# Kernel tuning notes

Hardware: AMD Instinct MI355X
Metric: run time of the kernel (lower is better)

The kernel has to match this reference:

```python
import jax, jax.numpy as jnp
import numpy as np

N = 100_000   # nodes
D = 128       # emb_size
E = 1_600_000 # edges (avg degree 16)
K = 64        # K1 (channel 0 pooling clusters)
LAYERS = 2


def _l2norm(x):
    # F.normalize(x, dim=-1, p=2) with eps=1e-12
    return x / jnp.maximum(jnp.linalg.norm(x, axis=-1, keepdims=True), 1e-12)


def setup_inputs() -> dict:
    key = jax.random.key(0)
    ks = jax.random.split(key, 9)
    return {
        "adj": jax.random.uniform(ks[0], (N,), dtype=jnp.float32),
        "edge_row": jax.random.randint(ks[1], (E,), 0, N),
        "edge_col": jax.random.randint(ks[2], (E,), 0, N),
        "edge_val": jax.random.uniform(ks[3], (E,), dtype=jnp.float32),
        "embedding": jax.random.normal(ks[4], (N, D), dtype=jnp.float32) * 0.02,
        "W_item0": jax.random.normal(ks[5], (D, D), dtype=jnp.float32) * 0.05,
        "W_item1": jax.random.normal(ks[6], (D, D), dtype=jnp.float32) * 0.05,
        "W_i1": jax.random.normal(ks[7], (D, D), dtype=jnp.float32) * 0.05,
        "W_i2": jax.random.normal(ks[8], (D, K), dtype=jnp.float32) * 0.05,
        "channel": 0,
    }


def reference(adj, edge_row, edge_col, edge_val, embedding,
              W_item0, W_item1, W_i1, W_i2, channel):
    n = adj.shape[0]

    def spmm(x):  # sparse [N,N] @ dense [N,D] via COO gather + segment_sum
        return jax.ops.segment_sum(edge_val[:, None] * x[edge_col], edge_row,
                                   num_segments=n)

    x = embedding
    final = [x]
    finalh = []
    for W in (W_item0, W_item1):  # structurally distinct per-layer weights
        x = spmm(x @ W)                                   # [N,D]
        H1 = jax.nn.relu(x @ W_i1 + x)                    # [N,D]
        H1 = jax.nn.softmax(H1 @ W_i2, axis=1)            # [N,K]
        h = H1.T * adj                                    # [K,N]
        h = h * (1.0 / (jnp.sum(h, axis=0) + 1e-8))       # column-normalize
        h = H1 @ (h @ x)                                  # [N,K]@[K,D] -> [N,D]
        x = h + x
        final.append(_l2norm(x))
        finalh.append(_l2norm(h))
    item_embeddings = sum(final) / (LAYERS + 1)
    hs = sum(finalh) / LAYERS
    return item_embeddings, hs
```

## Files before the change

kernel.cpp:

```cpp
#include <hip/hip_runtime.h>

constexpr int DD = 128;
constexpr int KK = 64;
constexpr int NBLK_C2 = 512;
constexpr int CH = 512;

typedef __attribute__((ext_vector_type(8))) short bf16x8;
typedef __attribute__((ext_vector_type(4))) float f32x4;

union U4 { unsigned u[4]; int4 i4; bf16x8 v; };

__device__ inline unsigned bf16_rne(float x) {
  unsigned u = __float_as_uint(x);
  u += 0x7fff + ((u >> 16) & 1);
  return u >> 16;
}
__device__ inline float bf16f(unsigned h) { return __uint_as_float(h << 16); }
__device__ inline void split2(float a, float b, unsigned& hi, unsigned& lo) {
  const unsigned h0 = bf16_rne(a), h1 = bf16_rne(b);
  const unsigned l0 = bf16_rne(a - bf16f(h0)), l1 = bf16_rne(b - bf16f(h1));
  hi = h0 | (h1 << 16);
  lo = l0 | (l1 << 16);
}

__global__ void k_prepW(const float* __restrict__ W, unsigned* __restrict__ Whi,
                        unsigned* __restrict__ Wlo) {
  const int id = blockIdx.x * 256 + threadIdx.x;
  const int j = id & 3, l = (id >> 2) & 63, t = (id >> 8) & 7, ks = id >> 11;
  const int k0 = 32 * ks + 8 * (l >> 4) + 2 * j;
  const int col = 16 * t + (l & 15);
  const float e0 = W[k0 * 128 + col], e1 = W[(k0 + 1) * 128 + col];
  unsigned hi, lo;
  split2(e0, e1, hi, lo);
  Whi[id] = hi;
  Wlo[id] = lo;
}

__global__ void k_prepWs(const float* __restrict__ W, unsigned* __restrict__ Wf) {
  const int id = blockIdx.x * 256 + threadIdx.x;
  const int j = id & 3, l = (id >> 2) & 63, t = (id >> 8) & 3, ks = id >> 10;
  const int k0 = 32 * ks + 8 * (l >> 4) + 2 * j;
  const int col = 16 * t + (l & 15);
  const unsigned h0 = bf16_rne(W[k0 * 64 + col]);
  const unsigned h1 = bf16_rne(W[(k0 + 1) * 64 + col]);
  Wf[id] = h0 | (h1 << 16);
}

__global__ void k_prepM(const float* __restrict__ M, unsigned* __restrict__ Mhi,
                        unsigned* __restrict__ Mlo) {
  const int id = blockIdx.x * 256 + threadIdx.x;
  const int j = id & 3, l = (id >> 2) & 63, t = (id >> 8) & 7, ks = id >> 11;
  const int k0 = 32 * ks + 8 * (l >> 4) + 2 * j;
  const int col = 16 * t + (l & 15);
  unsigned hi, lo;
  split2(M[k0 * 128 + col], M[(k0 + 1) * 128 + col], hi, lo);
  Mhi[id] = hi;
  Mlo[id] = lo;
}

__global__ __launch_bounds__(512) void k_gemm_mfma(const float* __restrict__ X,
                                                   const unsigned* __restrict__ Whi,
                                                   const unsigned* __restrict__ Wlo,
                                                   unsigned short* __restrict__ Yb,
                                                   int n) {
  __shared__ unsigned sb[2 * 8192];
  {
    const int t = threadIdx.x;
    uint4* d0 = (uint4*)sb;
    const uint4* s0 = (const uint4*)Whi;
#pragma unroll
    for (int i = 0; i < 4; ++i) d0[t + 512 * i] = s0[t + 512 * i];
    uint4* d1 = (uint4*)(sb + 8192);
    const uint4* s1 = (const uint4*)Wlo;
#pragma unroll
    for (int i = 0; i < 4; ++i) d1[t + 512 * i] = s1[t + 512 * i];
  }
  __syncthreads();
  const int wave = threadIdx.x >> 6, lane = threadIdx.x & 63;
  const int l15 = lane & 15, lhi = lane >> 4;
  const int row0 = blockIdx.x * 256 + wave * 32;
  if (row0 >= n) return;
  f32x4 acc[2][8];
#pragma unroll
  for (int rt = 0; rt < 2; ++rt)
#pragma unroll
    for (int t = 0; t < 8; ++t) acc[rt][t] = (f32x4){0.f, 0.f, 0.f, 0.f};
#pragma unroll
  for (int ks = 0; ks < 4; ++ks) {
    U4 ah[2], al[2];
#pragma unroll
    for (int rt = 0; rt < 2; ++rt) {
      int r = row0 + rt * 16 + l15;
      if (r >= n) r = n - 1;
      const float4 x0 = *(const float4*)&X[(size_t)r * DD + ks * 32 + lhi * 8];
      const float4 x1 = *(const float4*)&X[(size_t)r * DD + ks * 32 + lhi * 8 + 4];
      split2(x0.x, x0.y, ah[rt].u[0], al[rt].u[0]);
      split2(x0.z, x0.w, ah[rt].u[1], al[rt].u[1]);
      split2(x1.x, x1.y, ah[rt].u[2], al[rt].u[2]);
      split2(x1.z, x1.w, ah[rt].u[3], al[rt].u[3]);
    }
#pragma unroll
    for (int t = 0; t < 8; ++t) {
      U4 bh, bl;
      const int off = ((ks * 8 + t) * 64 + lane) * 4;
      bh.i4 = *(const int4*)&sb[off];
      bl.i4 = *(const int4*)&sb[8192 + off];
#pragma unroll
      for (int rt = 0; rt < 2; ++rt) {
        acc[rt][t] = __builtin_amdgcn_mfma_f32_16x16x32_bf16(ah[rt].v, bh.v, acc[rt][t], 0, 0, 0);
        acc[rt][t] = __builtin_amdgcn_mfma_f32_16x16x32_bf16(al[rt].v, bh.v, acc[rt][t], 0, 0, 0);
        acc[rt][t] = __builtin_amdgcn_mfma_f32_16x16x32_bf16(ah[rt].v, bl.v, acc[rt][t], 0, 0, 0);
      }
    }
  }
#pragma unroll
  for (int rt = 0; rt < 2; ++rt)
#pragma unroll
    for (int rr = 0; rr < 4; ++rr) {
      const int row = row0 + rt * 16 + lhi * 4 + rr;
      if (row < n) {
#pragma unroll
        for (int t = 0; t < 8; ++t)
          Yb[(size_t)row * DD + t * 16 + l15] =
              (unsigned short)bf16_rne(acc[rt][t][rr]);
      }
    }
}

__global__ void k_hist(const int* __restrict__ er, int* __restrict__ cnt, int E) {
  for (long e = (long)blockIdx.x * blockDim.x + threadIdx.x; e < E;
       e += (long)gridDim.x * blockDim.x)
    atomicAdd(&cnt[er[e]], 1);
}

__global__ __launch_bounds__(256) void k_chunksum(const int* __restrict__ cnt,
                                                  int* __restrict__ csum, int n) {
  const int c = blockIdx.x, t = threadIdx.x;
  const int i0 = c * CH + 2 * t;
  int s2 = 0;
  if (i0 < n) s2 += cnt[i0];
  if (i0 + 1 < n) s2 += cnt[i0 + 1];
#pragma unroll
  for (int off = 32; off >= 1; off >>= 1) s2 += __shfl_xor(s2, off);
  __shared__ int ws_[4];
  if ((t & 63) == 0) ws_[t >> 6] = s2;
  __syncthreads();
  if (t == 0) csum[c] = ws_[0] + ws_[1] + ws_[2] + ws_[3];
}

__global__ __launch_bounds__(256) void k_chunkscan(const int* __restrict__ csum,
                                                   int* __restrict__ coff, int nch) {
  __shared__ int s[256];
  const int t = threadIdx.x;
  const int v = (t < nch) ? csum[t] : 0;
  s[t] = v;
  __syncthreads();
  for (int off = 1; off < 256; off <<= 1) {
    const int u = (t >= off) ? s[t - off] : 0;
    __syncthreads();
    s[t] += u;
    __syncthreads();
  }
  coff[t] = s[t] - v;
}

__global__ __launch_bounds__(256) void k_rowptr(const int* __restrict__ cnt,
                                                const int* __restrict__ coff,
                                                int* __restrict__ rowptr,
                                                int n, int E) {
  const int c = blockIdx.x, t = threadIdx.x;
  const int i0 = c * CH + 2 * t, i1 = i0 + 1;
  const int v0 = (i0 < n) ? cnt[i0] : 0;
  const int v1 = (i1 < n) ? cnt[i1] : 0;
  __shared__ int s[256];
  const int s2 = v0 + v1;
  s[t] = s2;
  __syncthreads();
  for (int off = 1; off < 256; off <<= 1) {
    const int u = (t >= off) ? s[t - off] : 0;
    __syncthreads();
    s[t] += u;
    __syncthreads();
  }
  const int excl = s[t] - s2 + coff[c];
  if (i0 < n) rowptr[i0] = excl;
  if (i1 < n) rowptr[i1] = excl + v0;
  if (c == 0 && t == 0) rowptr[n] = E;
}

__global__ void k_scatter(const int* __restrict__ er, const int* __restrict__ ec,
                          const float* __restrict__ ev,
                          const int* __restrict__ rowptr, int* __restrict__ cur,
                          int2* __restrict__ erec, int E, int n) {
  const int rng = blockIdx.x & 7;
  const int g = blockIdx.x >> 3;
  const long e_lo = (long)g * E / 256;
  const long e_hi = (long)(g + 1) * E / 256;
  const int r_lo = (int)((long)rng * n / 8);
  const int r_hi = (int)((long)(rng + 1) * n / 8);
  for (long e = e_lo + threadIdx.x; e < e_hi; e += 256) {
    const int r = er[e];
    if (r >= r_lo && r < r_hi) {
      const int pos = rowptr[r] + atomicAdd(&cur[r], 1);
      erec[pos] = make_int2(ec[e], __float_as_int(ev[e]));
    }
  }
}

__global__ __launch_bounds__(256) void k_spmm_csr(const int* __restrict__ rowptr,
                                                  const int2* __restrict__ erec,
                                                  const unsigned* __restrict__ Yb,
                                                  float* __restrict__ Xo, int n) {
  const int lane = threadIdx.x & 63;
  const int c0 = 2 * lane;
  const long gw = (long)blockIdx.x * 4 + (threadIdx.x >> 6);
  const long nw = (long)gridDim.x * 4;
  for (long row = gw; row < n; row += nw) {
    const int b = rowptr[row], e2 = rowptr[row + 1];
    float a0 = 0.f, a1 = 0.f, b0 = 0.f, b1 = 0.f;
    float c00 = 0.f, c1 = 0.f, d0 = 0.f, d1 = 0.f;
    int e = b;
    for (; e + 4 <= e2; e += 4) {
      const int2 r0 = erec[e], r1 = erec[e + 1];
      const int2 r2 = erec[e + 2], r3 = erec[e + 3];
      const unsigned q0 = Yb[(size_t)r0.x * (DD / 2) + lane];
      const unsigned q1 = Yb[(size_t)r1.x * (DD / 2) + lane];
      const unsigned q2 = Yb[(size_t)r2.x * (DD / 2) + lane];
      const unsigned q3 = Yb[(size_t)r3.x * (DD / 2) + lane];
      const float v0 = __int_as_float(r0.y), v1 = __int_as_float(r1.y);
      const float v2 = __int_as_float(r2.y), v3 = __int_as_float(r3.y);
      a0 = fmaf(v0, __uint_as_float(q0 << 16), a0);
      a1 = fmaf(v0, __uint_as_float(q0 & 0xffff0000u), a1);
      b0 = fmaf(v1, __uint_as_float(q1 << 16), b0);
      b1 = fmaf(v1, __uint_as_float(q1 & 0xffff0000u), b1);
      c00 = fmaf(v2, __uint_as_float(q2 << 16), c00);
      c1 = fmaf(v2, __uint_as_float(q2 & 0xffff0000u), c1);
      d0 = fmaf(v3, __uint_as_float(q3 << 16), d0);
      d1 = fmaf(v3, __uint_as_float(q3 & 0xffff0000u), d1);
    }
    for (; e + 2 <= e2; e += 2) {
      const int2 r0 = erec[e], r1 = erec[e + 1];
      const float v0 = __int_as_float(r0.y), v1 = __int_as_float(r1.y);
      const unsigned q0 = Yb[(size_t)r0.x * (DD / 2) + lane];
      const unsigned q1 = Yb[(size_t)r1.x * (DD / 2) + lane];
      a0 = fmaf(v0, __uint_as_float(q0 << 16), a0);
      a1 = fmaf(v0, __uint_as_float(q0 & 0xffff0000u), a1);
      b0 = fmaf(v1, __uint_as_float(q1 << 16), b0);
      b1 = fmaf(v1, __uint_as_float(q1 & 0xffff0000u), b1);
    }
    if (e < e2) {
      const int2 r0 = erec[e];
      const float v = __int_as_float(r0.y);
      const unsigned q = Yb[(size_t)r0.x * (DD / 2) + lane];
      a0 = fmaf(v, __uint_as_float(q << 16), a0);
      a1 = fmaf(v, __uint_as_float(q & 0xffff0000u), a1);
    }
    *(float2*)&Xo[(size_t)row * DD + c0] =
        make_float2((a0 + b0) + (c00 + d0), (a1 + b1) + (c1 + d1));
  }
}

__global__ __launch_bounds__(512) void k_c1_mfma(const float* __restrict__ X,
                                                 const unsigned* __restrict__ W1hi,
                                                 const unsigned* __restrict__ W1lo,
                                                 const unsigned* __restrict__ W2f,
                                                 const float* __restrict__ adj,
                                                 float* __restrict__ H1g,
                                                 float* __restrict__ trow, int n) {
  __shared__ unsigned s1[2 * 8192];
  __shared__ unsigned s2[4096];
  __shared__ unsigned h1s[8 * 16 * 68];
  {
    const int t = threadIdx.x;
    uint4* d0 = (uint4*)s1;
    const uint4* sA = (const uint4*)W1hi;
    const uint4* sB = (const uint4*)W1lo;
#pragma unroll
    for (int i = 0; i < 4; ++i) d0[t + 512 * i] = sA[t + 512 * i];
    uint4* d1 = (uint4*)(s1 + 8192);
#pragma unroll
    for (int i = 0; i < 4; ++i) d1[t + 512 * i] = sB[t + 512 * i];
    uint4* d2 = (uint4*)s2;
    const uint4* sC = (const uint4*)W2f;
#pragma unroll
    for (int i = 0; i < 2; ++i) d2[t + 512 * i] = sC[t + 512 * i];
  }
  __syncthreads();
  const int wave = threadIdx.x >> 6, lane = threadIdx.x & 63;
  const int l15 = lane & 15, lhi = lane >> 4;
  unsigned* __restrict__ h1w = h1s + wave * (16 * 68);
  const int row0 = blockIdx.x * 128 + wave * 16;
  if (row0 >= n) return;

  U4 ah[4], al[4];
#pragma unroll
  for (int ks = 0; ks < 4; ++ks) {
    int r = row0 + l15;
    if (r >= n) r = n - 1;
    const float4 x0 = *(const float4*)&X[(size_t)r * DD + ks * 32 + lhi * 8];
    const float4 x1 = *(const float4*)&X[(size_t)r * DD + ks * 32 + lhi * 8 + 4];
    split2(x0.x, x0.y, ah[ks].u[0], al[ks].u[0]);
    split2(x0.z, x0.w, ah[ks].u[1], al[ks].u[1]);
    split2(x1.x, x1.y, ah[ks].u[2], al[ks].u[2]);
    split2(x1.z, x1.w, ah[ks].u[3], al[ks].u[3]);
  }
  f32x4 acc1[8];
#pragma unroll
  for (int t = 0; t < 8; ++t) acc1[t] = (f32x4){0.f, 0.f, 0.f, 0.f};
#pragma unroll
  for (int ks = 0; ks < 4; ++ks) {
#pragma unroll
    for (int t = 0; t < 8; ++t) {
      U4 bh, bl;
      const int off = ((ks * 8 + t) * 64 + lane) * 4;
      bh.i4 = *(const int4*)&s1[off];
      bl.i4 = *(const int4*)&s1[8192 + off];
      acc1[t] = __builtin_amdgcn_mfma_f32_16x16x32_bf16(ah[ks].v, bh.v, acc1[t], 0, 0, 0);
      acc1[t] = __builtin_amdgcn_mfma_f32_16x16x32_bf16(al[ks].v, bh.v, acc1[t], 0, 0, 0);
      acc1[t] = __builtin_amdgcn_mfma_f32_16x16x32_bf16(ah[ks].v, bl.v, acc1[t], 0, 0, 0);
    }
  }

  unsigned short* __restrict__ h16 = (unsigned short*)h1w;
#pragma unroll
  for (int rr = 0; rr < 4; ++rr) {
    int row = row0 + 4 * lhi + rr;
    if (row >= n) row = n - 1;
    const float* __restrict__ xr = X + (size_t)row * DD;
#pragma unroll
    for (int t = 0; t < 8; ++t) {
      float v = acc1[t][rr] + xr[16 * t + l15];
      v = fmaxf(v, 0.f);
      h16[(4 * lhi + rr) * 136 + 16 * t + l15] = (unsigned short)bf16_rne(v);
    }
  }

  f32x4 acc3[4];
#pragma unroll
  for (int t = 0; t < 4; ++t) acc3[t] = (f32x4){0.f, 0.f, 0.f, 0.f};
#pragma unroll
  for (int ks = 0; ks < 4; ++ks) {
    U4 a3;
    a3.i4 = *(const int4*)&h1w[l15 * 68 + ks * 16 + lhi * 4];
#pragma unroll
    for (int t = 0; t < 4; ++t) {
      U4 b3;
      b3.i4 = *(const int4*)&s2[((ks * 4 + t) * 64 + lane) * 4];
      acc3[t] = __builtin_amdgcn_mfma_f32_16x16x32_bf16(a3.v, b3.v, acc3[t], 0, 0, 0);
    }
  }

#pragma unroll
  for (int rr = 0; rr < 4; ++rr) {
    const int row = row0 + 4 * lhi + rr;
    float z0 = acc3[0][rr], z1 = acc3[1][rr], z2 = acc3[2][rr], z3 = acc3[3][rr];
    float m = fmaxf(fmaxf(z0, z1), fmaxf(z2, z3));
#pragma unroll
    for (int off = 8; off >= 1; off >>= 1) m = fmaxf(m, __shfl_xor(m, off));
    const float p0 = expf(z0 - m), p1 = expf(z1 - m);
    const float p2 = expf(z2 - m), p3 = expf(z3 - m);
    float s = p0 + p1 + p2 + p3;
#pragma unroll
    for (int off = 8; off >= 1; off >>= 1) s += __shfl_xor(s, off);
    const float inv = 1.0f / s;
    if (row < n) {
      float* __restrict__ hr = H1g + (size_t)row * KK;
      hr[l15] = p0 * inv;
      hr[16 + l15] = p1 * inv;
      hr[32 + l15] = p2 * inv;
      hr[48 + l15] = p3 * inv;
      if (l15 == 0) {
        const float a = adj[row];
        trow[row] = a / (a + 1e-8f);
      }
    }
  }
}

__global__ __launch_bounds__(1024, 4) void k_c2(const float* __restrict__ X,
                                                const float* __restrict__ trow,
                                                const float* __restrict__ H1g,
                                                float* __restrict__ Mpart, int n) {
  __shared__ float cmb[3 * 4 * 16 * 2 * 64];
  const int t = threadIdx.x;
  const int wave = t >> 6, lane = t & 63;
  const int rg = wave >> 2, kg = wave & 3;
  const int kb = kg * 16;
  const int d0 = 2 * lane;
  float macc[16][2];
#pragma unroll
  for (int j = 0; j < 16; ++j) { macc[j][0] = 0.f; macc[j][1] = 0.f; }
  const int bx = blockIdx.x;
  for (long row = (long)bx + 512L * rg; row < n; row += 2048L) {
    const int r = __builtin_amdgcn_readfirstlane((int)row);
    const float tr = trow[r];
    const float2 xv = *(const float2*)&X[(size_t)r * DD + d0];
    const float px0 = tr * xv.x, px1 = tr * xv.y;
    const float* __restrict__ hrow = H1g + (size_t)r * KK + kb;
#pragma unroll
    for (int j = 0; j < 16; ++j) {
      const float hj = hrow[j];
      macc[j][0] = fmaf(hj, px0, macc[j][0]);
      macc[j][1] = fmaf(hj, px1, macc[j][1]);
    }
  }
  if (rg > 0) {
    float* __restrict__ dst = cmb + ((rg - 1) * 4 + kg) * (16 * 2 * 64);
#pragma unroll
    for (int j = 0; j < 16; ++j) {
      dst[(2 * j + 0) * 64 + lane] = macc[j][0];
      dst[(2 * j + 1) * 64 + lane] = macc[j][1];
    }
  }
  __syncthreads();
  if (rg == 0) {
#pragma unroll
    for (int g = 0; g < 3; ++g) {
      const float* __restrict__ src = cmb + (g * 4 + kg) * (16 * 2 * 64);
#pragma unroll
      for (int j = 0; j < 16; ++j) {
        macc[j][0] += src[(2 * j + 0) * 64 + lane];
        macc[j][1] += src[(2 * j + 1) * 64 + lane];
      }
    }
    float* __restrict__ mp = Mpart + (size_t)bx * (KK * DD);
#pragma unroll
    for (int j = 0; j < 16; ++j)
      *(float2*)&mp[(kb + j) * DD + d0] = make_float2(macc[j][0], macc[j][1]);
  }
}

__global__ void k_dred1(const float* __restrict__ Mpart, float* __restrict__ Mp2) {
  const int j = blockIdx.x * blockDim.x + threadIdx.x;
  const int i = j & (KK * DD - 1);
  const int c = j >> 13;
  float s = 0.f;
#pragma unroll
  for (int q = 0; q < 16; ++q)
    s += Mpart[(size_t)(c * 16 + q) * (KK * DD) + i];
  Mp2[(size_t)c * (KK * DD) + i] = s;
}

__global__ void k_dred2(const float* __restrict__ Mp2, float* __restrict__ Mg) {
  const int i = blockIdx.x * blockDim.x + threadIdx.x;
  float s = 0.f;
#pragma unroll
  for (int c = 0; c < 32; ++c) s += Mp2[(size_t)c * (KK * DD) + i];
  Mg[i] = s;
}

__global__ __launch_bounds__(512) void k_fin_mfma(const float* __restrict__ H1g,
                                                  const unsigned* __restrict__ Mhi,
                                                  const unsigned* __restrict__ Mlo,
                                                  const float* __restrict__ emb,
                                                  float* __restrict__ Xb,
                                                  float* __restrict__ out,
                                                  int n, int first) {
  __shared__ unsigned sm[2 * 4096];
  {
    const int t = threadIdx.x;
    uint4* d0 = (uint4*)sm;
    const uint4* s0 = (const uint4*)Mhi;
#pragma unroll
    for (int i = 0; i < 2; ++i) d0[t + 512 * i] = s0[t + 512 * i];
    uint4* d1 = (uint4*)(sm + 4096);
    const uint4* s1 = (const uint4*)Mlo;
#pragma unroll
    for (int i = 0; i < 2; ++i) d1[t + 512 * i] = s1[t + 512 * i];
  }
  __syncthreads();
  const int wave = threadIdx.x >> 6, lane = threadIdx.x & 63;
  const int l15 = lane & 15, lhi = lane >> 4;
  const size_t hoff = (size_t)n * DD;
  const int row0 = blockIdx.x * 128 + wave * 16;
  if (row0 >= n) return;

  U4 ah[2], al[2];
  {
    int ra = row0 + l15;
    if (ra >= n) ra = n - 1;
    const float* __restrict__ hp = H1g + (size_t)ra * KK;
#pragma unroll
    for (int ks = 0; ks < 2; ++ks) {
      const float4 x0 = *(const float4*)&hp[ks * 32 + lhi * 8];
      const float4 x1 = *(const float4*)&hp[ks * 32 + lhi * 8 + 4];
      split2(x0.x, x0.y, ah[ks].u[0], al[ks].u[0]);
      split2(x0.z, x0.w, ah[ks].u[1], al[ks].u[1]);
      split2(x1.x, x1.y, ah[ks].u[2], al[ks].u[2]);
      split2(x1.z, x1.w, ah[ks].u[3], al[ks].u[3]);
    }
  }
  f32x4 acc[8];
#pragma unroll
  for (int t = 0; t < 8; ++t) acc[t] = (f32x4){0.f, 0.f, 0.f, 0.f};
#pragma unroll
  for (int ks = 0; ks < 2; ++ks) {
#pragma unroll
    for (int t = 0; t < 8; ++t) {
      U4 bh, bl;
      const int off = ((ks * 8 + t) * 64 + lane) * 4;
      bh.i4 = *(const int4*)&sm[off];
      bl.i4 = *(const int4*)&sm[4096 + off];
      acc[t] = __builtin_amdgcn_mfma_f32_16x16x32_bf16(ah[ks].v, bh.v, acc[t], 0, 0, 0);
      acc[t] = __builtin_amdgcn_mfma_f32_16x16x32_bf16(al[ks].v, bh.v, acc[t], 0, 0, 0);
      acc[t] = __builtin_amdgcn_mfma_f32_16x16x32_bf16(ah[ks].v, bl.v, acc[t], 0, 0, 0);
    }
  }
#pragma unroll
  for (int rr = 0; rr < 4; ++rr) {
    const int row = row0 + 4 * lhi + rr;
    const int rc = (row < n) ? row : (n - 1);
    float hh[8], xx[8];
    float sh = 0.f, sx = 0.f;
#pragma unroll
    for (int t = 0; t < 8; ++t) {
      const float xv = Xb[(size_t)rc * DD + 16 * t + l15];
      hh[t] = acc[t][rr];
      xx[t] = hh[t] + xv;
      sh = fmaf(hh[t], hh[t], sh);
      sx = fmaf(xx[t], xx[t], sx);
    }
#pragma unroll
    for (int off = 8; off >= 1; off >>= 1) {
      sh += __shfl_xor(sh, off);
      sx += __shfl_xor(sx, off);
    }
    const float ih = 0.5f / fmaxf(sqrtf(sh), 1e-12f);
    const float ix = (1.0f / 3.0f) / fmaxf(sqrtf(sx), 1e-12f);
    if (row < n) {
#pragma unroll
      for (int t = 0; t < 8; ++t) {
        const size_t oi = (size_t)row * DD + 16 * t + l15;
        Xb[oi] = xx[t];
        float ci, ch;
        if (first) {
          ci = emb[oi] * (1.0f / 3.0f);
          ch = 0.f;
        } else {
          ci = out[oi];
          ch = out[hoff + oi];
        }
        out[oi] = ci + xx[t] * ix;
        out[hoff + oi] = ch + hh[t] * ih;
      }
    }
  }
}

extern "C" void kernel_launch(void* const* d_in, const int* in_sizes, int n_in,
                              void* d_out, int out_size, void* d_ws, size_t ws_size,
                              hipStream_t stream) {
  const float* adj  = (const float*)d_in[0];
  const int*   erow = (const int*)d_in[1];
  const int*   ecol = (const int*)d_in[2];
  const float* eval = (const float*)d_in[3];
  const float* emb  = (const float*)d_in[4];
  const float* W0   = (const float*)d_in[5];
  const float* W1   = (const float*)d_in[6];
  const float* Wi1  = (const float*)d_in[7];
  const float* Wi2  = (const float*)d_in[8];
  const int n = in_sizes[0];
  const int E = in_sizes[1];
  float* out = (float*)d_out;

  float* xb    = (float*)d_ws;
  float* yb    = xb + (size_t)n * DD;
  unsigned short* Ybf = (unsigned short*)yb;
  float* H1g   = yb + (size_t)n * (DD / 2);
  float* Mpart = H1g + (size_t)n * KK;
  float* Mp2   = Mpart + (size_t)NBLK_C2 * KK * DD;
  float* Mg    = Mp2 + (size_t)32 * KK * DD;
  int*   cnt    = (int*)(Mg + KK * DD);
  int*   rowptr = cnt + n;
  int*   csum   = rowptr + n + 4;
  int*   coff   = csum + 256;
  int2*  erec   = (int2*)(coff + 256);
  float* trow   = (float*)(erec + E);
  unsigned* w0hi  = (unsigned*)(trow + n);
  unsigned* w0lo  = w0hi + 8192;
  unsigned* w1hi_ = w0lo + 8192;
  unsigned* w1lo_ = w1hi_ + 8192;
  unsigned* wi1hi = w1lo_ + 8192;
  unsigned* wi1lo = wi1hi + 8192;
  unsigned* wi2f  = wi1lo + 8192;
  unsigned* mhi   = wi2f + 4096;
  unsigned* mlo   = mhi + 4096;

  const int NCH = (n + CH - 1) / CH;

  k_prepW<<<32, 256, 0, stream>>>(W0, w0hi, w0lo);
  k_prepW<<<32, 256, 0, stream>>>(W1, w1hi_, w1lo_);
  k_prepW<<<32, 256, 0, stream>>>(Wi1, wi1hi, wi1lo);
  k_prepWs<<<16, 256, 0, stream>>>(Wi2, wi2f);

  hipMemsetAsync(cnt, 0, (size_t)n * sizeof(int), stream);
  k_hist<<<2048, 256, 0, stream>>>(erow, cnt, E);
  k_chunksum<<<NCH, 256, 0, stream>>>(cnt, csum, n);
  k_chunkscan<<<1, 256, 0, stream>>>(csum, coff, NCH);
  k_rowptr<<<NCH, 256, 0, stream>>>(cnt, coff, rowptr, n, E);
  hipMemsetAsync(cnt, 0, (size_t)n * sizeof(int), stream);
  k_scatter<<<2048, 256, 0, stream>>>(erow, ecol, eval, rowptr, cnt, erec, E, n);

  const int g_gm  = (n + 255) / 256;
  const int g_c1m = (n + 127) / 128;
  const int g_fin = (n + 127) / 128;

  for (int L = 0; L < 2; ++L) {
    const unsigned* Whi = (L == 0) ? w0hi : w1hi_;
    const unsigned* Wlo = (L == 0) ? w0lo : w1lo_;
    const float* Xin = (L == 0) ? emb : xb;
    k_gemm_mfma<<<g_gm, 512, 0, stream>>>(Xin, Whi, Wlo, Ybf, n);
    k_spmm_csr<<<2048, 256, 0, stream>>>(rowptr, erec, (const unsigned*)Ybf, xb, n);
    k_c1_mfma<<<g_c1m, 512, 0, stream>>>(xb, wi1hi, wi1lo, wi2f, adj, H1g, trow, n);
    k_c2<<<NBLK_C2, 1024, 0, stream>>>(xb, trow, H1g, Mpart, n);
    k_dred1<<<1024, 256, 0, stream>>>(Mpart, Mp2);
    k_dred2<<<32, 256, 0, stream>>>(Mp2, Mg);
    k_prepM<<<16, 256, 0, stream>>>(Mg, mhi, mlo);
    k_fin_mfma<<<g_fin, 512, 0, stream>>>(H1g, mhi, mlo, emb, xb, out, n, (L == 0) ? 1 : 0);
  }
}
```

Baseline: 711.0 us.

## Build CSR via two-pass shared-memory bucketing and deepen SpMM unroll to 8

Replaces the 8-way row-range-filtered atomic scatter with a two-pass bucket sort. The first pass bins edges into 512-row buckets in shared memory and flushes them in chunks to a scratch buffer aliased onto xb. The second pass places each bucket's edges into their final CSR slots using shared-memory atomics. This cuts the repeated reads of the edge arrays and the scattered global atomics, at the cost of an extra pass and a bit-packed column/local-row encoding that assumes columns fit in 20 bits. The SpMM inner loop is also unrolled to 8 independent gathers to raise memory-level parallelism, which uses more registers.

Measured after the change: 720.5 us. No clear change (+1.3%).

```diff
diff --git a/kernel.cpp b/kernel.cpp
--- a/kernel.cpp
+++ b/kernel.cpp
@@ -4,6 +4,8 @@
 constexpr int KK = 64;
 constexpr int NBLK_C2 = 512;
 constexpr int CH = 512;
+constexpr int NBK = 256;
+constexpr int BCAP = 32;
 
 typedef __attribute__((ext_vector_type(8))) short bf16x8;
 typedef __attribute__((ext_vector_type(4))) float f32x4;
@@ -188,22 +190,88 @@
   if (c == 0 && t == 0) rowptr[n] = E;
 }
 
-__global__ void k_scatter(const int* __restrict__ er, const int* __restrict__ ec,
-                          const float* __restrict__ ev,
-                          const int* __restrict__ rowptr, int* __restrict__ cur,
-                          int2* __restrict__ erec, int E, int n) {
-  const int rng = blockIdx.x & 7;
-  const int g = blockIdx.x >> 3;
-  const long e_lo = (long)g * E / 256;
-  const long e_hi = (long)(g + 1) * E / 256;
-  const int r_lo = (int)((long)rng * n / 8);
-  const int r_hi = (int)((long)(rng + 1) * n / 8);
-  for (long e = e_lo + threadIdx.x; e < e_hi; e += 256) {
-    const int r = er[e];
-    if (r >= r_lo && r < r_hi) {
-      const int pos = rowptr[r] + atomicAdd(&cur[r], 1);
-      erec[pos] = make_int2(ec[e], __float_as_int(ev[e]));
-    }
+__global__ __launch_bounds__(256) void k_bucketA(const int* __restrict__ er,
+                                                 const int* __restrict__ ec,
+                                                 const float* __restrict__ ev,
+                                                 const int* __restrict__ rowptr,
+                                                 int* __restrict__ gcur,
+                                                 int2* __restrict__ gbuf,
+                                                 int E, int nbk) {
+  __shared__ int2 buf[NBK * BCAP];
+  __shared__ int cnt[NBK];
+  const int t = threadIdx.x;
+  for (int i = t; i < NBK; i += 256) cnt[i] = 0;
+  __syncthreads();
+  const long e_lo = (long)blockIdx.x * E / 512;
+  const long e_hi = (long)(blockIdx.x + 1) * E / 512;
+  for (long s = e_lo; s < e_hi; s += 2048) {
+    const long s_end = (s + 2048 < e_hi) ? (s + 2048) : e_hi;
+    unsigned pend = 0;
+#pragma unroll
+    for (int k = 0; k < 8; ++k) {
+      const long e = s + t + 256 * k;
+      if (e < s_end) {
+        const int r = er[e];
+        const int b = r >> 9;
+        const int p = atomicAdd(&cnt[b], 1);
+        if (p < BCAP)
+          buf[b * BCAP + p] = make_int2(ec[e] | ((r & 511) << 20), __float_as_int(ev[e]));
+        else
+          pend |= 1u << k;
+      }
+    }
+    __syncthreads();
+    if (t < nbk) {
+      const int m = min(cnt[t], BCAP);
+      if (m > 0) {
+        const int base = rowptr[t << 9] + atomicAdd(&gcur[t], m);
+        for (int i = 0; i < m; ++i) gbuf[base + i] = buf[t * BCAP + i];
+      }
+      cnt[t] = 0;
+    }
+    __syncthreads();
+    while (pend) {
+      const int k = __ffs(pend) - 1;
+      pend &= pend - 1;
+      const long e = s + t + 256 * k;
+      const int r = er[e];
+      const int b = r >> 9;
+      const int2 rec = make_int2(ec[e] | ((r & 511) << 20), __float_as_int(ev[e]));
+      const int p = atomicAdd(&cnt[b], 1);
+      if (p < BCAP) {
+        buf[b * BCAP + p] = rec;
+      } else {
+        const int base = rowptr[b << 9] + atomicAdd(&gcur[b], 1);
+        gbuf[base] = rec;
+      }
+    }
+  }
+  __syncthreads();
+  if (t < nbk) {
+    const int m = min(cnt[t], BCAP);
+    if (m > 0) {
+      const int base = rowptr[t << 9] + atomicAdd(&gcur[t], m);
+      for (int i = 0; i < m; ++i) gbuf[base + i] = buf[t * BCAP + i];
+    }
+  }
+}
+
+__global__ __launch_bounds__(512) void k_bucketB(const int2* __restrict__ gbuf,
+                                                 const int* __restrict__ rowptr,
+                                                 int2* __restrict__ erec, int n) {
+  __shared__ int cur[512];
+  const int b = blockIdx.x, t = threadIdx.x;
+  cur[t] = 0;
+  __syncthreads();
+  const int r_lo = b << 9;
+  const int r_hi = (r_lo + 512 < n) ? (r_lo + 512) : n;
+  const int g_lo = rowptr[r_lo], g_hi = rowptr[r_hi];
+  for (int i = g_lo + t; i < g_hi; i += 512) {
+    const int2 rec = gbuf[i];
+    const int rl = ((unsigned)rec.x) >> 20;
+    const int col = rec.x & 0xFFFFF;
+    const int pos = rowptr[r_lo + rl] + atomicAdd(&cur[rl], 1);
+    erec[pos] = make_int2(col, rec.y);
   }
 }
 
@@ -217,46 +285,44 @@
   const long nw = (long)gridDim.x * 4;
   for (long row = gw; row < n; row += nw) {
     const int b = rowptr[row], e2 = rowptr[row + 1];
-    float a0 = 0.f, a1 = 0.f, b0 = 0.f, b1 = 0.f;
-    float c00 = 0.f, c1 = 0.f, d0 = 0.f, d1 = 0.f;
+    float a0[8], a1[8];
+#pragma unroll
+    for (int i = 0; i < 8; ++i) { a0[i] = 0.f; a1[i] = 0.f; }
     int e = b;
-    for (; e + 4 <= e2; e += 4) {
+    for (; e + 8 <= e2; e += 8) {
+      int2 rr[8];
+      unsigned qq[8];
+#pragma unroll
+      for (int i = 0; i < 8; ++i) rr[i] = erec[e + i];
+#pragma unroll
+      for (int i = 0; i < 8; ++i) qq[i] = Yb[(size_t)rr[i].x * (DD / 2) + lane];
+#pragma unroll
+      for (int i = 0; i < 8; ++i) {
+        const float v = __int_as_float(rr[i].y);
+        a0[i] = fmaf(v, __uint_as_float(qq[i] << 16), a0[i]);
+        a1[i] = fmaf(v, __uint_as_float(qq[i] & 0xffff0000u), a1[i]);
+      }
+    }
+    for (; e + 2 <= e2; e += 2) {
       const int2 r0 = erec[e], r1 = erec[e + 1];
-      const int2 r2 = erec[e + 2], r3 = erec[e + 3];
       const unsigned q0 = Yb[(size_t)r0.x * (DD / 2) + lane];
       const unsigned q1 = Yb[(size_t)r1.x * (DD / 2) + lane];
-      const unsigned q2 = Yb[(size_t)r2.x * (DD / 2) + lane];
-      const unsigned q3 = Yb[(size_t)r3.x * (DD / 2) + lane];
       const float v0 = __int_as_float(r0.y), v1 = __int_as_float(r1.y);
-      const float v2 = __int_as_float(r2.y), v3 = __int_as_float(r3.y);
-      a0 = fmaf(v0, __uint_as_float(q0 << 16), a0);
-      a1 = fmaf(v0, __uint_as_float(q0 & 0xffff0000u), a1);
-      b0 = fmaf(v1, __uint_as_float(q1 << 16), b0);
-      b1 = fmaf(v1, __uint_as_float(q1 & 0xffff0000u), b1);
-      c00 = fmaf(v2, __uint_as_float(q2 << 16), c00);
-      c1 = fmaf(v2, __uint_as_float(q2 & 0xffff0000u), c1);
-      d0 = fmaf(v3, __uint_as_float(q3 << 16), d0);
-      d1 = fmaf(v3, __uint_as_float(q3 & 0xffff0000u), d1);
-    }
-    for (; e + 2 <= e2; e += 2) {
-      const int2 r0 = erec[e], r1 = erec[e + 1];
-      const float v0 = __int_as_float(r0.y), v1 = __int_as_float(r1.y);
-      const unsigned q0 = Yb[(size_t)r0.x * (DD / 2) + lane];
-      const unsigned q1 = Yb[(size_t)r1.x * (DD / 2) + lane];
-      a0 = fmaf(v0, __uint_as_float(q0 << 16), a0);
-      a1 = fmaf(v0, __uint_as_float(q0 & 0xffff0000u), a1);
-      b0 = fmaf(v1, __uint_as_float(q1 << 16), b0);
-      b1 = fmaf(v1, __uint_as_float(q1 & 0xffff0000u), b1);
+      a0[0] = fmaf(v0, __uint_as_float(q0 << 16), a0[0]);
+      a1[0] = fmaf(v0, __uint_as_float(q0 & 0xffff0000u), a1[0]);
+      a0[1] = fmaf(v1, __uint_as_float(q1 << 16), a0[1]);
+      a1[1] = fmaf(v1, __uint_as_float(q1 & 0xffff0000u), a1[1]);
     }
     if (e < e2) {
       const int2 r0 = erec[e];
       const float v = __int_as_float(r0.y);
       const unsigned q = Yb[(size_t)r0.x * (DD / 2) + lane];
-      a0 = fmaf(v, __uint_as_float(q << 16), a0);
-      a1 = fmaf(v, __uint_as_float(q & 0xffff0000u), a1);
-    }
-    *(float2*)&Xo[(size_t)row * DD + c0] =
-        make_float2((a0 + b0) + (c00 + d0), (a1 + b1) + (c1 + d1));
+      a0[0] = fmaf(v, __uint_as_float(q << 16), a0[0]);
+      a1[0] = fmaf(v, __uint_as_float(q & 0xffff0000u), a1[0]);
+    }
+    const float s0 = ((a0[0] + a0[1]) + (a0[2] + a0[3])) + ((a0[4] + a0[5]) + (a0[6] + a0[7]));
+    const float s1 = ((a1[0] + a1[1]) + (a1[2] + a1[3])) + ((a1[4] + a1[5]) + (a1[6] + a1[7]));
+    *(float2*)&Xo[(size_t)row * DD + c0] = make_float2(s0, s1);
   }
 }
 
@@ -585,8 +651,10 @@
   unsigned* wi2f  = wi1lo + 8192;
   unsigned* mhi   = wi2f + 4096;
   unsigned* mlo   = mhi + 4096;
+  int2* gbuf = (int2*)xb;
 
   const int NCH = (n + CH - 1) / CH;
+  const int nbk = (n + 511) >> 9;
 
   k_prepW<<<32, 256, 0, stream>>>(W0, w0hi, w0lo);
   k_prepW<<<32, 256, 0, stream>>>(W1, w1hi_, w1lo_);
@@ -598,8 +666,9 @@
   k_chunksum<<<NCH, 256, 0, stream>>>(cnt, csum, n);
   k_chunkscan<<<1, 256, 0, stream>>>(csum, coff, NCH);
   k_rowptr<<<NCH, 256, 0, stream>>>(cnt, coff, rowptr, n, E);
-  hipMemsetAsync(cnt, 0, (size_t)n * sizeof(int), stream);
-  k_scatter<<<2048, 256, 0, stream>>>(erow, ecol, eval, rowptr, cnt, erec, E, n);
+  hipMemsetAsync(csum, 0, 256 * sizeof(int), stream);
+  k_bucketA<<<512, 256, 0, stream>>>(erow, ecol, eval, rowptr, csum, gbuf, E, nbk);
+  k_bucketB<<<nbk, 512, 0, stream>>>(gbuf, rowptr, erec, n);
 
   const int g_gm  = (n + 255) / 256;
   const int g_c1m = (n + 127) / 128;
```
